# Kernel optimization log

Hardware: AMD Instinct MI355X
Metric: run time of the kernel (lower is better)

The kernel has to match this reference:

```python
import jax, jax.numpy as jnp
import numpy as np

B, S, D, H = 2, 2048, 2048, 16
HD = D // H


def setup_inputs() -> dict:
    key = jax.random.key(0)
    ks = jax.random.split(key, 11)
    scale = 1.0 / np.sqrt(D)
    causal = jnp.tril(jnp.ones((S, S), dtype=bool))
    attention_mask = jnp.broadcast_to(causal, (B, H, S, S))
    return {
        "queries": jax.random.normal(ks[0], (B, S, D), dtype=jnp.float32),
        "keys": jax.random.normal(ks[1], (B, S, D), dtype=jnp.float32),
        "values": jax.random.normal(ks[2], (B, S, D), dtype=jnp.float32),
        "attention_mask": attention_mask,
        "wq": jax.random.normal(ks[3], (D, D), dtype=jnp.float32) * scale,
        "bq": jax.random.normal(ks[4], (D,), dtype=jnp.float32) * 0.01,
        "wk": jax.random.normal(ks[5], (D, D), dtype=jnp.float32) * scale,
        "bk": jax.random.normal(ks[6], (D,), dtype=jnp.float32) * 0.01,
        "wv": jax.random.normal(ks[7], (D, D), dtype=jnp.float32) * scale,
        "bv": jax.random.normal(ks[8], (D,), dtype=jnp.float32) * 0.01,
        "wo": jax.random.normal(ks[9], (D, D), dtype=jnp.float32) * scale,
        "bo": jax.random.normal(ks[10], (D,), dtype=jnp.float32) * 0.01,
    }


def _split_heads(x):
    # (B, S, D) -> (B, H, S, HD)
    b, s, _ = x.shape
    return x.reshape(b, s, H, HD).transpose(0, 2, 1, 3)


def reference(queries, keys, values, attention_mask, wq, bq, wk, bk, wv, bv, wo, bo):
    # Linear layers (torch convention: x @ W.T + b)
    q = _split_heads(queries @ wq.T + bq)   # (B, H, S, HD)
    k = _split_heads(keys @ wk.T + bk)
    v = _split_heads(values @ wv.T + bv)

    inv_sqrt_d = 1.0 / jnp.sqrt(jnp.asarray(HD, dtype=q.dtype))
    scores = jnp.einsum('bhqd,bhkd->bhqk', q, k) * inv_sqrt_d  # (B, H, S, S)
    scores = jnp.where(attention_mask, scores, jnp.asarray(-jnp.inf, dtype=scores.dtype))
    probs = jax.nn.softmax(scores, axis=-1)
    out = jnp.einsum('bhqk,bhkd->bhqd', probs, v)              # (B, H, S, HD)

    out = out.transpose(0, 2, 1, 3).reshape(queries.shape[0], queries.shape[1], D)
    return out @ wo.T + bo
```

## Files before the change

kernel.cpp:

```cpp
#include <hip/hip_runtime.h>
#include <hip/hip_bf16.h>

typedef unsigned short u16;
typedef __bf16 bf16x8 __attribute__((ext_vector_type(8)));
typedef short  short8 __attribute__((ext_vector_type(8)));
typedef float  f32x4  __attribute__((ext_vector_type(4)));
typedef u16    u16x4  __attribute__((ext_vector_type(4)));

#define BB 2
#define SS 2048
#define DD 2048
#define HH 16
#define HDIM 128
#define MM (BB * SS)
#define KSCALE 0.12752039505554602f

static __device__ __forceinline__ f32x4 mfma16(short8 a, short8 b, f32x4 c) {
    return __builtin_amdgcn_mfma_f32_16x16x32_bf16(
        __builtin_bit_cast(bf16x8, a), __builtin_bit_cast(bf16x8, b), c, 0, 0, 0);
}

static __device__ __forceinline__ u16 f2bf(float f) {
    union { float f; unsigned u; } v; v.f = f;
    unsigned r = v.u + 0x7fffu + ((v.u >> 16) & 1u);
    return (u16)(r >> 16);
}

static __device__ __forceinline__ uint4 pack8(float4 a, float4 b) {
    uint4 o;
    o.x = (unsigned)f2bf(a.x) | ((unsigned)f2bf(a.y) << 16);
    o.y = (unsigned)f2bf(a.z) | ((unsigned)f2bf(a.w) << 16);
    o.z = (unsigned)f2bf(b.x) | ((unsigned)f2bf(b.y) << 16);
    o.w = (unsigned)f2bf(b.z) | ((unsigned)f2bf(b.w) << 16);
    return o;
}

static __device__ __forceinline__ void gload_lds16(const u16* g, u16* l) {
    __builtin_amdgcn_global_load_lds(
        (const __attribute__((address_space(1))) unsigned int*)g,
        (__attribute__((address_space(3))) unsigned int*)l, 16, 0, 0);
}

__global__ __launch_bounds__(256) void conv_all(
    const float* __restrict__ q, const float* __restrict__ k, const float* __restrict__ v,
    const float* __restrict__ wq, const float* __restrict__ wk,
    const float* __restrict__ wv, const float* __restrict__ wo,
    u16* __restrict__ out)
{
    constexpr int n1 = MM * DD / 8;
    constexpr int nw = DD * DD / 8;
    constexpr int total = 3 * n1 + 4 * nw;
    const int stride = gridDim.x * blockDim.x;
    for (int i = blockIdx.x * blockDim.x + threadIdx.x; i < total; i += stride) {
        const float* s; int j = i; float sc = 1.f;
        if (j < n1)            { s = q; }
        else if (j < 2 * n1)   { s = k;  j -= n1; }
        else if (j < 3 * n1)   { s = v;  j -= 2 * n1; }
        else {
            j -= 3 * n1;
            if (j < nw)        { s = wq; sc = KSCALE; }
            else if (j < 2*nw) { s = wk; j -= nw; }
            else if (j < 3*nw) { s = wv; j -= 2 * nw; }
            else               { s = wo; j -= 3 * nw; }
        }
        const float4* sp = (const float4*)s + (size_t)j * 2;
        float4 a = sp[0], bb2 = sp[1];
        a.x *= sc; a.y *= sc; a.z *= sc; a.w *= sc;
        bb2.x *= sc; bb2.y *= sc; bb2.z *= sc; bb2.w *= sc;
        ((uint4*)out)[i] = pack8(a, bb2);
    }
}

__global__ __launch_bounds__(256, 3) void gemm_qkv(
    const u16* __restrict__ A0, const u16* __restrict__ W0,
    const float* __restrict__ bq, const float* __restrict__ bk,
    const float* __restrict__ bv, u16* __restrict__ C0)
{
    __shared__ u16 S[128 * 132];
    u16* Al = S;
    u16* Bl = S + 4096;

    const int z = blockIdx.z;
    const u16* A  = A0 + (size_t)z * MM * DD;
    const u16* Wb = W0 + (size_t)z * DD * DD;
    const float* bias = (z == 0) ? bq : (z == 1 ? bk : bv);
    const float bsc = (z == 0) ? KSCALE : 1.f;

    const int tid = threadIdx.x;
    const int lane = tid & 63;
    const int lg = lane >> 4, li = lane & 15;
    const int wid = tid >> 6;
    const int brow = blockIdx.x * 128, bcol = blockIdx.y * 128;
    const int wm = wid >> 1, wn = wid & 1;

    const int srow = tid >> 2;
    const int scol = (tid & 3) * 8;

    const f32x4 zero = {0.f, 0.f, 0.f, 0.f};
    f32x4 acc[4][4];
#pragma unroll
    for (int i = 0; i < 4; ++i)
#pragma unroll
        for (int j = 0; j < 4; ++j) acc[i][j] = zero;

    const u16* aptr = A  + (size_t)(brow + srow) * DD + scol;
    const u16* bptr = Wb + (size_t)(bcol + srow) * DD + scol;
    const size_t half = (size_t)64 * DD;

    for (int kt = 0; kt < DD; kt += 32) {
        gload_lds16(aptr + kt,        &Al[tid * 8]);
        gload_lds16(aptr + half + kt, &Al[2048 + tid * 8]);
        gload_lds16(bptr + kt,        &Bl[tid * 8]);
        gload_lds16(bptr + half + kt, &Bl[2048 + tid * 8]);
        __syncthreads();

        short8 af[4], bf[4];
#pragma unroll
        for (int mi = 0; mi < 4; ++mi)
            af[mi] = *(const short8*)(&Al[(wm * 64 + mi * 16 + li) * 32 + lg * 8]);
#pragma unroll
        for (int ni = 0; ni < 4; ++ni)
            bf[ni] = *(const short8*)(&Bl[(wn * 64 + ni * 16 + li) * 32 + lg * 8]);
#pragma unroll
        for (int mi = 0; mi < 4; ++mi)
#pragma unroll
            for (int ni = 0; ni < 4; ++ni)
                acc[mi][ni] = mfma16(af[mi], bf[ni], acc[mi][ni]);
        __syncthreads();
    }

    if (z == 2) {
        u16* Cl = S;
#pragma unroll
        for (int ni = 0; ni < 4; ++ni) {
            const int cc = wn * 64 + ni * 16 + li;
            const float bvv = bias[bcol + cc];
#pragma unroll
            for (int mi = 0; mi < 4; ++mi)
#pragma unroll
                for (int r = 0; r < 4; ++r) {
                    const int rr = wm * 64 + mi * 16 + lg * 4 + r;
                    Cl[cc * 132 + rr] = f2bf(acc[mi][ni][r] + bvv);
                }
        }
        __syncthreads();
        const int row = tid >> 1;
        const int hcol = (tid & 1) * 64;
        u16* dst = C0 + (size_t)2 * MM * DD + (size_t)(bcol + row) * MM + brow + hcol;
#pragma unroll
        for (int c = 0; c < 8; ++c)
            *(short8*)(dst + c * 8) = *(const short8*)(&Cl[row * 132 + hcol + c * 8]);
    } else {
        u16* Cp = C0 + (size_t)z * MM * DD;
#pragma unroll
        for (int ni = 0; ni < 4; ++ni) {
            const int col = bcol + wn * 64 + ni * 16 + li;
            const float bvv = bias[col] * bsc;
#pragma unroll
            for (int mi = 0; mi < 4; ++mi)
#pragma unroll
                for (int r = 0; r < 4; ++r) {
                    const int row = brow + wm * 64 + mi * 16 + lg * 4 + r;
                    Cp[(size_t)row * DD + col] = f2bf(acc[mi][ni][r] + bvv);
                }
        }
    }
}

__global__ __launch_bounds__(256) void gemm_out(
    const u16* __restrict__ A, const u16* __restrict__ Wb,
    const float* __restrict__ bias, float* __restrict__ Cp)
{
    __shared__ u16 Al[128 * 32];
    __shared__ u16 Bl[128 * 32];

    const int tid = threadIdx.x;
    const int lane = tid & 63;
    const int lg = lane >> 4, li = lane & 15;
    const int wid = tid >> 6;
    const int brow = blockIdx.x * 128, bcol = blockIdx.y * 128;
    const int wm = wid >> 1, wn = wid & 1;

    const int srow = tid >> 2;
    const int scol = (tid & 3) * 8;

    const f32x4 zero = {0.f, 0.f, 0.f, 0.f};
    f32x4 acc[4][4];
#pragma unroll
    for (int i = 0; i < 4; ++i)
#pragma unroll
        for (int j = 0; j < 4; ++j) acc[i][j] = zero;

    const u16* aptr = A  + (size_t)(brow + srow) * DD + scol;
    const u16* bptr = Wb + (size_t)(bcol + srow) * DD + scol;
    const size_t half = (size_t)64 * DD;

    for (int kt = 0; kt < DD; kt += 32) {
        gload_lds16(aptr + kt,        &Al[tid * 8]);
        gload_lds16(aptr + half + kt, &Al[2048 + tid * 8]);
        gload_lds16(bptr + kt,        &Bl[tid * 8]);
        gload_lds16(bptr + half + kt, &Bl[2048 + tid * 8]);
        __syncthreads();

        short8 af[4], bf[4];
#pragma unroll
        for (int mi = 0; mi < 4; ++mi)
            af[mi] = *(const short8*)(&Al[(wm * 64 + mi * 16 + li) * 32 + lg * 8]);
#pragma unroll
        for (int ni = 0; ni < 4; ++ni)
            bf[ni] = *(const short8*)(&Bl[(wn * 64 + ni * 16 + li) * 32 + lg * 8]);
#pragma unroll
        for (int mi = 0; mi < 4; ++mi)
#pragma unroll
            for (int ni = 0; ni < 4; ++ni)
                acc[mi][ni] = mfma16(af[mi], bf[ni], acc[mi][ni]);
        __syncthreads();
    }

#pragma unroll
    for (int ni = 0; ni < 4; ++ni) {
        const int col = bcol + wn * 64 + ni * 16 + li;
        const float bvv = bias[col];
#pragma unroll
        for (int mi = 0; mi < 4; ++mi)
#pragma unroll
            for (int r = 0; r < 4; ++r) {
                const int row = brow + wm * 64 + mi * 16 + lg * 4 + r;
                Cp[(size_t)row * DD + col] = acc[mi][ni][r] + bvv;
            }
    }
}

__global__ __launch_bounds__(256) void flash_attn(
    const u16* __restrict__ Q, const u16* __restrict__ Kp,
    const u16* __restrict__ Vt, u16* __restrict__ O)
{
    constexpr int SP = 72;
    __shared__ u16 lds[16384 + 4 * 32 * SP];
    u16* Kl = lds;
    u16* Vl = lds + 8192;
    u16* Pl = lds + 16384;

    const int tid = threadIdx.x;
    const int wid = tid >> 6, lane = tid & 63;
    const int lg = lane >> 4, li = lane & 15;
    const int qt = (int)gridDim.x - 1 - (int)blockIdx.x;
    const int h = blockIdx.y, b = blockIdx.z;
    const int nt = 2 * qt + 2;
    const int qbase = qt * 128 + wid * 32;

    const int rK0 = tid >> 4, wK0 = tid & 15;
    const int bK0 = ((wK0 * 16) ^ ((rK0 & 7) << 4)) >> 1;
    const int rV0 = tid >> 3, wV0 = tid & 7;
    const int bV0 = ((wV0 * 16) ^ ((rV0 & 7) << 4)) >> 1;
    const u16* kbase = Kp + (size_t)(b * SS + rK0) * DD + h * HDIM + bK0;
    const u16* vbase = Vt + (size_t)(h * HDIM + rV0) * MM + b * SS + bV0;

    short8 qf[4][2];
    {
        const u16* qp0 = Q + (size_t)(b * SS + qbase + li) * DD + h * HDIM + lg * 8;
#pragma unroll
        for (int qh = 0; qh < 2; ++qh)
#pragma unroll
            for (int s = 0; s < 4; ++s)
                qf[s][qh] = *(const short8*)(qp0 + (size_t)qh * 16 * DD + s * 32);
    }

    const f32x4 zero = {0.f, 0.f, 0.f, 0.f};
    float m_r[2], l_r[2];
    m_r[0] = m_r[1] = -__builtin_inff();
    l_r[0] = l_r[1] = 0.f;
    f32x4 accO[8][2];
#pragma unroll
    for (int d = 0; d < 8; ++d) accO[d][0] = accO[d][1] = zero;

    for (int j = 0; j < nt; ++j) {
#pragma unroll
        for (int i_ = 0; i_ < 4; ++i_) {
            gload_lds16(kbase + (size_t)(j * 64 + i_ * 16) * DD, &Kl[(i_ * 256 + tid) * 8]);
            gload_lds16(vbase + (size_t)(i_ * 32) * MM + j * 64, &Vl[(i_ * 256 + tid) * 8]);
        }
        __syncthreads();

        if (j * 64 <= qbase + 31) {
            f32x4 accS[4][2];
#pragma unroll
            for (int nb = 0; nb < 4; ++nb) accS[nb][0] = accS[nb][1] = zero;
            __builtin_amdgcn_s_setprio(1);
#pragma unroll
            for (int s = 0; s < 4; ++s) {
#pragma unroll
                for (int nb = 0; nb < 4; ++nb) {
                    const int R = nb * 16 + li;
                    const int e = ((s * 64 + lg * 16) ^ ((R & 7) << 4)) >> 1;
                    short8 kf = *(const short8*)(&Kl[R * 128 + e]);
#pragma unroll
                    for (int qh = 0; qh < 2; ++qh)
                        accS[nb][qh] = mfma16(kf, qf[s][qh], accS[nb][qh]);
                }
            }
            __builtin_amdgcn_s_setprio(0);

            const bool domask = (j * 64 + 63 > qbase);
            float rmax[2];
            rmax[0] = rmax[1] = -__builtin_inff();
#pragma unroll
            for (int nb = 0; nb < 4; ++nb)
#pragma unroll
                for (int qh = 0; qh < 2; ++qh)
#pragma unroll
                    for (int r = 0; r < 4; ++r) {
                        float t = accS[nb][qh][r];
                        if (domask && (j * 64 + nb * 16 + lg * 4 + r >
                                       qbase + qh * 16 + li)) t = -__builtin_inff();
                        accS[nb][qh][r] = t;
                        rmax[qh] = fmaxf(rmax[qh], t);
                    }
#pragma unroll
            for (int qh = 0; qh < 2; ++qh) {
                rmax[qh] = fmaxf(rmax[qh], __shfl_xor(rmax[qh], 16, 64));
                rmax[qh] = fmaxf(rmax[qh], __shfl_xor(rmax[qh], 32, 64));
            }

            const bool need = (rmax[0] - m_r[0] > 11.5f) || (rmax[1] - m_r[1] > 11.5f);
            if (__any(need)) {
#pragma unroll
                for (int qh = 0; qh < 2; ++qh) {
                    const float mn = fmaxf(m_r[qh], rmax[qh]);
                    const float sf = exp2f(m_r[qh] - mn);
                    m_r[qh] = mn;
                    l_r[qh] *= sf;
#pragma unroll
                    for (int mb = 0; mb < 8; ++mb)
#pragma unroll
                        for (int r = 0; r < 4; ++r) accO[mb][qh][r] *= sf;
                }
            }

            float ls[2] = {0.f, 0.f};
#pragma unroll
            for (int nb = 0; nb < 4; ++nb)
#pragma unroll
                for (int qh = 0; qh < 2; ++qh)
#pragma unroll
                    for (int r = 0; r < 4; ++r) {
                        const float e = exp2f(accS[nb][qh][r] - m_r[qh]);
                        accS[nb][qh][r] = e;
                        ls[qh] += e;
                    }
#pragma unroll
            for (int qh = 0; qh < 2; ++qh) {
                ls[qh] += __shfl_xor(ls[qh], 16, 64);
                ls[qh] += __shfl_xor(ls[qh], 32, 64);
                l_r[qh] += ls[qh];
            }

#pragma unroll
            for (int nb = 0; nb < 4; ++nb)
#pragma unroll
                for (int qh = 0; qh < 2; ++qh) {
                    u16x4 pk;
                    pk.x = f2bf(accS[nb][qh][0]);
                    pk.y = f2bf(accS[nb][qh][1]);
                    pk.z = f2bf(accS[nb][qh][2]);
                    pk.w = f2bf(accS[nb][qh][3]);
                    *(u16x4*)(&Pl[(wid * 32 + qh * 16 + li) * SP + nb * 16 + lg * 4]) = pk;
                }

            __builtin_amdgcn_s_setprio(1);
#pragma unroll
            for (int s2 = 0; s2 < 2; ++s2) {
                short8 pf[2];
#pragma unroll
                for (int qh = 0; qh < 2; ++qh)
                    pf[qh] = *(const short8*)(&Pl[(wid * 32 + qh * 16 + li) * SP +
                                                  s2 * 32 + lg * 8]);
#pragma unroll
                for (int mb = 0; mb < 8; ++mb) {
                    const int R2 = mb * 16 + li;
                    const int e2 = ((s2 * 64 + lg * 16) ^ ((R2 & 7) << 4)) >> 1;
                    short8 vf = *(const short8*)(&Vl[R2 * 64 + e2]);
#pragma unroll
                    for (int qh = 0; qh < 2; ++qh)
                        accO[mb][qh] = mfma16(vf, pf[qh], accO[mb][qh]);
                }
            }
            __builtin_amdgcn_s_setprio(0);
        }
        __syncthreads();
    }

    {
        float linv[2] = {1.f / l_r[0], 1.f / l_r[1]};
        u16* Wl = lds + wid * 4096;
#pragma unroll
        for (int mb = 0; mb < 8; ++mb)
#pragma unroll
            for (int qh = 0; qh < 2; ++qh) {
                const int q_l = qh * 16 + li;
                const int dbase = mb * 16 + lg * 4;
                u16x4 pk;
                pk.x = f2bf(accO[mb][qh][0] * linv[qh]);
                pk.y = f2bf(accO[mb][qh][1] * linv[qh]);
                pk.z = f2bf(accO[mb][qh][2] * linv[qh]);
                pk.w = f2bf(accO[mb][qh][3] * linv[qh]);
                *(u16x4*)(&Wl[q_l * 128 + (dbase ^ ((q_l & 7) << 4))]) = pk;
            }
        const int q_l = lane >> 1;
        const int d0 = (lane & 1) * 64;
        u16* op = O + (size_t)(b * SS + qt * 128 + wid * 32 + q_l) * DD + h * HDIM + d0;
#pragma unroll
        for (int c = 0; c < 8; ++c) {
            short8 vv = *(const short8*)(&Wl[q_l * 128 + ((d0 + c * 8) ^ ((q_l & 7) << 4))]);
            *(short8*)(op + c * 8) = vv;
        }
    }
}

extern "C" void kernel_launch(void* const* d_in, const int* in_sizes, int n_in,
                              void* d_out, int out_size, void* d_ws, size_t ws_size,
                              hipStream_t stream)
{
    const float* queries = (const float*)d_in[0];
    const float* keys    = (const float*)d_in[1];
    const float* values  = (const float*)d_in[2];
    const float* wq = (const float*)d_in[4];
    const float* bq = (const float*)d_in[5];
    const float* wk = (const float*)d_in[6];
    const float* bk = (const float*)d_in[7];
    const float* wv = (const float*)d_in[8];
    const float* bv = (const float*)d_in[9];
    const float* wo = (const float*)d_in[10];
    const float* bo = (const float*)d_in[11];

    const int NMD = MM * DD;
    const int NWW = DD * DD;

    u16* qb  = (u16*)d_ws;
    u16* wqb = qb  + (size_t)3 * NMD;
    u16* wob = wqb + (size_t)3 * NWW;
    u16* qw  = wob + (size_t)NWW;
    u16* aw  = qw  + (size_t)3 * NMD;
    (void)in_sizes; (void)n_in; (void)out_size; (void)ws_size;

    dim3 blk(256);
    dim3 gridC(2048);
    dim3 gridQKV(MM / 128, DD / 128, 3);
    dim3 gridO(MM / 128, DD / 128);
    dim3 gridA(SS / 128, HH, BB);

    conv_all<<<gridC, blk, 0, stream>>>(queries, keys, values, wq, wk, wv, wo, qb);
    gemm_qkv<<<gridQKV, blk, 0, stream>>>(qb, wqb, bq, bk, bv, qw);
    flash_attn<<<gridA, blk, 0, stream>>>(qw, qw + (size_t)NMD, qw + (size_t)2 * NMD, aw);
    gemm_out<<<gridO, blk, 0, stream>>>(aw, wob, bo, (float*)d_out);
}
```

Baseline: 400.8 us.

## Split causal attention KV range into chunks and add a combine kernel

Long causal query tiles are split into up to four KV chunks of 8 tiles each, so 16 uneven per-head work items become 40 more even ones. Short tiles still write their final output directly. Chunked tiles write unnormalized bf16 partial outputs plus row max and sum to workspace buffers that are no longer needed at that point. A new combine kernel merges them with log-sum-exp weights. This aims to cut the causal load-imbalance tail, at the cost of an extra launch, partial-result traffic, and bf16 rounding of the partials.

```diff
diff --git a/kernel.cpp b/kernel.cpp
--- a/kernel.cpp
+++ b/kernel.cpp
@@ -24,6 +24,11 @@
     union { float f; unsigned u; } v; v.f = f;
     unsigned r = v.u + 0x7fffu + ((v.u >> 16) & 1u);
     return (u16)(r >> 16);
+}
+
+static __device__ __forceinline__ float bf2f(u16 v) {
+    union { unsigned u; float f; } t; t.u = ((unsigned)v) << 16;
+    return t.f;
 }
 
 static __device__ __forceinline__ uint4 pack8(float4 a, float4 b) {
@@ -233,7 +238,8 @@
 
 __global__ __launch_bounds__(256) void flash_attn(
     const u16* __restrict__ Q, const u16* __restrict__ Kp,
-    const u16* __restrict__ Vt, u16* __restrict__ O)
+    const u16* __restrict__ Vt, u16* __restrict__ O,
+    u16* __restrict__ PartO, float* __restrict__ PartML)
 {
     constexpr int SP = 72;
     __shared__ u16 lds[16384 + 4 * 32 * SP];
@@ -244,9 +250,16 @@
     const int tid = threadIdx.x;
     const int wid = tid >> 6, lane = tid & 63;
     const int lg = lane >> 4, li = lane & 15;
-    const int qt = (int)gridDim.x - 1 - (int)blockIdx.x;
     const int h = blockIdx.y, b = blockIdx.z;
-    const int nt = 2 * qt + 2;
+
+    const int f = 39 - (int)blockIdx.x;
+    int qt, ch;
+    if (f < 4)       { qt = f;               ch = 0; }
+    else if (f < 12) { int g = f - 4;  qt = 4  + (g >> 1); ch = g & 1; }
+    else if (f < 24) { int g = f - 12; qt = 8  + g / 3;    ch = g % 3; }
+    else             { int g = f - 24; qt = 12 + (g >> 2); ch = g & 3; }
+    const int j0 = ch * 8;
+    const int j1 = min(j0 + 8, 2 * qt + 2);
     const int qbase = qt * 128 + wid * 32;
 
     const int rK0 = tid >> 4, wK0 = tid & 15;
@@ -274,7 +287,7 @@
 #pragma unroll
     for (int d = 0; d < 8; ++d) accO[d][0] = accO[d][1] = zero;
 
-    for (int j = 0; j < nt; ++j) {
+    for (int j = j0; j < j1; ++j) {
 #pragma unroll
         for (int i_ = 0; i_ < 4; ++i_) {
             gload_lds16(kbase + (size_t)(j * 64 + i_ * 16) * DD, &Kl[(i_ * 256 + tid) * 8]);
@@ -390,7 +403,29 @@
         __syncthreads();
     }
 
-    {
+    if (f >= 4) {
+        const int pslot = (b * HH + h) * 36 + (f - 4);
+        u16* po = PartO + (size_t)pslot * 16384;
+#pragma unroll
+        for (int mb = 0; mb < 8; ++mb)
+#pragma unroll
+            for (int qh = 0; qh < 2; ++qh) {
+                const int q_g = wid * 32 + qh * 16 + li;
+#pragma unroll
+                for (int r = 0; r < 4; ++r) {
+                    const int d = mb * 16 + lg * 4 + r;
+                    po[d * 128 + q_g] = f2bf(accO[mb][qh][r]);
+                }
+            }
+        if (lg == 0) {
+            float* ml = PartML + (size_t)pslot * 256;
+#pragma unroll
+            for (int qh = 0; qh < 2; ++qh) {
+                ml[wid * 32 + qh * 16 + li]       = m_r[qh];
+                ml[128 + wid * 32 + qh * 16 + li] = l_r[qh];
+            }
+        }
+    } else {
         float linv[2] = {1.f / l_r[0], 1.f / l_r[1]};
         u16* Wl = lds + wid * 4096;
 #pragma unroll
@@ -414,6 +449,61 @@
             short8 vv = *(const short8*)(&Wl[q_l * 128 + ((d0 + c * 8) ^ ((q_l & 7) << 4))]);
             *(short8*)(op + c * 8) = vv;
         }
+    }
+}
+
+__global__ __launch_bounds__(256) void attn_combine(
+    const u16* __restrict__ PartO, const float* __restrict__ PartML,
+    u16* __restrict__ O)
+{
+    const int qt = 4 + (int)blockIdx.x;
+    const int h = blockIdx.y, b = blockIdx.z;
+    const int nch = qt / 4 + 1;
+    int f0m4;
+    if (qt < 8)       f0m4 = (qt - 4) * 2;
+    else if (qt < 12) f0m4 = 8 + (qt - 8) * 3;
+    else              f0m4 = 20 + (qt - 12) * 4;
+    const int pbase = (b * HH + h) * 36 + f0m4;
+
+    const int tid = threadIdx.x;
+    const int q = tid & 127;
+    const int d0 = (tid >> 7) * 64;
+
+    float mc[4], lc[4];
+#pragma unroll
+    for (int c = 0; c < 4; ++c) {
+        if (c < nch) {
+            mc[c] = PartML[(size_t)(pbase + c) * 256 + q];
+            lc[c] = PartML[(size_t)(pbase + c) * 256 + 128 + q];
+        } else { mc[c] = -__builtin_inff(); lc[c] = 0.f; }
+    }
+    float M = fmaxf(fmaxf(mc[0], mc[1]), fmaxf(mc[2], mc[3]));
+    float wc[4], L = 0.f;
+#pragma unroll
+    for (int c = 0; c < 4; ++c) { wc[c] = exp2f(mc[c] - M); L += wc[c] * lc[c]; }
+    const float Linv = 1.f / L;
+
+    float acc[64];
+#pragma unroll
+    for (int i = 0; i < 64; ++i) acc[i] = 0.f;
+#pragma unroll
+    for (int c = 0; c < 4; ++c) {
+        if (c < nch) {
+            const float w = wc[c] * Linv;
+            const u16* po = PartO + (size_t)(pbase + c) * 16384 + q;
+#pragma unroll
+            for (int i = 0; i < 64; ++i)
+                acc[i] += w * bf2f(po[(size_t)(d0 + i) * 128]);
+        }
+    }
+
+    u16* op = O + (size_t)(b * SS + qt * 128 + q) * DD + h * HDIM + d0;
+#pragma unroll
+    for (int j = 0; j < 8; ++j) {
+        short8 vv;
+#pragma unroll
+        for (int e = 0; e < 8; ++e) vv[e] = (short)f2bf(acc[j * 8 + e]);
+        *(short8*)(op + j * 8) = vv;
     }
 }
 
@@ -441,16 +531,21 @@
     u16* wob = wqb + (size_t)3 * NWW;
     u16* qw  = wob + (size_t)NWW;
     u16* aw  = qw  + (size_t)3 * NMD;
+    u16*   partO  = qb;
+    float* partML = (float*)wqb;
     (void)in_sizes; (void)n_in; (void)out_size; (void)ws_size;
 
     dim3 blk(256);
     dim3 gridC(2048);
     dim3 gridQKV(MM / 128, DD / 128, 3);
     dim3 gridO(MM / 128, DD / 128);
-    dim3 gridA(SS / 128, HH, BB);
+    dim3 gridA(40, HH, BB);
+    dim3 gridX(12, HH, BB);
 
     conv_all<<<gridC, blk, 0, stream>>>(queries, keys, values, wq, wk, wv, wo, qb);
     gemm_qkv<<<gridQKV, blk, 0, stream>>>(qb, wqb, bq, bk, bv, qw);
-    flash_attn<<<gridA, blk, 0, stream>>>(qw, qw + (size_t)NMD, qw + (size_t)2 * NMD, aw);
+    flash_attn<<<gridA, blk, 0, stream>>>(qw, qw + (size_t)NMD, qw + (size_t)2 * NMD, aw,
+                                          partO, partML);
+    attn_combine<<<gridX, blk, 0, stream>>>(partO, partML, aw);
     gemm_out<<<gridO, blk, 0, stream>>>(aw, wob, bo, (float*)d_out);
 }
```

Measured after the change: 349.1 us. 12.9% less time.
